# Optimization experiments

Measured on AMD Instinct MI355X. Metric: run time of the kernel, lower is better.

## Reference

```python
import jax, jax.numpy as jnp
import numpy as np

N = 50000   # nodes
E = 400000  # edges
R = 35      # num_relations
B = 12      # num_bases
C = 128     # hidden_conv_dim (heads=1)
T = 4       # node types: load, gen, load_gen, ext
HL = 38     # hidden_lin_dim
OUT = 2


def setup_inputs() -> dict:
    key = jax.random.key(0)
    ks = jax.random.split(key, 24)
    s = 0.1  # param scale
    inp = {
        'x': jax.random.normal(ks[0], (N, 2), jnp.float32),
        'edge_index': jax.random.randint(ks[1], (2, E), 0, N, jnp.int32),
        'edge_type': jax.random.randint(ks[2], (E,), 0, R, jnp.int32),
        'edge_attr': jax.random.normal(ks[3], (E, 2), jnp.float32),
        'node_type': jax.random.randint(ks[4], (N,), 0, T, jnp.int32),
        'basis': jax.random.normal(ks[5], (B, 2, C), jnp.float32) * s,
        'att_rel': jax.random.normal(ks[6], (R, B), jnp.float32) * s,
        'q_att': jax.random.normal(ks[7], (C, 1), jnp.float32) * s,
        'k_att': jax.random.normal(ks[8], (C, 1), jnp.float32) * s,
        'e_att': jax.random.normal(ks[9], (C, 1), jnp.float32) * s,
        'lin_edge_W': jax.random.normal(ks[10], (2, C), jnp.float32) * s,
        'conv_bias': jax.random.normal(ks[11], (C,), jnp.float32) * s,
        'lin0_W': jax.random.normal(ks[12], (T, C, HL), jnp.float32) * s,
        'lin0_b': jax.random.normal(ks[13], (T, HL), jnp.float32) * s,
        'lin1_W': jax.random.normal(ks[14], (T, HL, HL), jnp.float32) * s,
        'lin1_b': jax.random.normal(ks[15], (T, HL), jnp.float32) * s,
        'lin2_W': jax.random.normal(ks[16], (T, HL, HL), jnp.float32) * s,
        'lin2_b': jax.random.normal(ks[17], (T, HL), jnp.float32) * s,
        'fin_W': jax.random.normal(ks[18], (T, HL, OUT), jnp.float32) * s,
        'fin_b': jax.random.normal(ks[19], (T, OUT), jnp.float32) * s,
    }
    return inp


def _segment_softmax(alpha, dst, n):
    # PyG softmax: max is detached, eps=1e-16 on the denominator
    amax = jax.lax.stop_gradient(jax.ops.segment_max(alpha, dst, num_segments=n))
    ex = jnp.exp(alpha - amax[dst])
    den = jax.ops.segment_sum(ex, dst, num_segments=n) + 1e-16
    return ex / den[dst]


def _per_type_linear(xv, W, b, t):
    # apply node-type-specific Linear: [N,d] x [T,d,h] -> pick row type
    y = jnp.einsum('nd,tdh->nth', xv, W)              # [N,T,h]
    y = jnp.take_along_axis(y, t[:, None, None], axis=1)[:, 0]
    return y + b[t]


def reference(x, edge_index, edge_type, edge_attr, node_type,
              basis, att_rel, q_att, k_att, e_att, lin_edge_W, conv_bias,
              lin0_W, lin0_b, lin1_W, lin1_b, lin2_W, lin2_b, fin_W, fin_b):
    n = x.shape[0]
    src, dst = edge_index[0], edge_index[1]
    # RGATConv with basis decomposition: per-relation weight [R, in=2, C]
    w = jnp.einsum('rb,bio->rio', att_rel, basis)
    w_e = w[edge_type]                                 # [E,2,C] edge gather
    out_i = jnp.einsum('ei,eic->ec', x[dst], w_e)      # [E,C]
    out_j = jnp.einsum('ei,eic->ec', x[src], w_e)      # [E,C]
    ke = (edge_attr @ lin_edge_W) @ e_att              # [E,1]
    alpha = out_i @ q_att + out_j @ k_att + ke         # additive self-attention
    alpha = jax.nn.leaky_relu(alpha, 0.2)
    alpha = _segment_softmax(alpha, dst, n)            # across-relation segment softmax
    msg = alpha * out_j                                # heads=1 -> [E,C]
    agg = jax.ops.segment_sum(msg, dst, num_segments=n) + conv_bias
    h = jax.nn.leaky_relu(agg, 0.2)                    # forward activation (dropout: eval)
    t = node_type
    h = _per_type_linear(jax.nn.relu(h), lin0_W, lin0_b, t)
    h = _per_type_linear(jax.nn.relu(h), lin1_W, lin1_b, t)
    h = _per_type_linear(jax.nn.relu(h), lin2_W, lin2_b, t)
    out = _per_type_linear(h, fin_W, fin_b, t)         # [N,2]
    # load nodes (type 0): second output passes through abs
    load_out = jnp.concatenate([out[:, :1], jnp.abs(out[:, 1:2])], axis=1)
    return jnp.where((t == 0)[:, None], load_out, out)
```

## Files before the change

### kernel.cpp

```cpp
#include <hip/hip_runtime.h>
#include <math.h>

#define N_NODES 50000
#define N_EDGES 400000
#define R_REL   35
#define B_BASES 12
#define C_DIM   128
#define HL_DIM  38
#define RI2     70
#define BI2     24
#define NP      50304
#define NB_HIST 196
#define NBUCK   786
#define EPB     1024
#define NEB     391
#define CAP     704

#define OFF_WQ     8960
#define OFF_WK     9030
#define OFF_LE     9100
#define OFF_META   9104
#define OFF_HBLK   9120
#define OFF_PERM   10688
#define OFF_INV    60688
#define OFF_ECUR   110992
#define OFF_EREC   111780
#define OFF_W0P    2325156
#define OFF_W1P    2345636
#define OFF_W2P    2351716

#define ST    0
#define SB    4760
#define HH    0
#define Y0T   0
#define Y1T   3264
#define Y2T   0
#define SM_DINV 8192
#define SM_FW   8256
#define SM_FB   8332
#define LDS_FLOATS 8334

__global__ __launch_bounds__(256) void k_hist(const int* __restrict__ node_type,
                                              float* __restrict__ ws) {
    int b = blockIdx.x, tid = threadIdx.x;
    if (b >= NB_HIST) {
        for (int i = tid; i < NBUCK; i += 256) ((int*)(ws + OFF_ECUR))[i] = 0;
        return;
    }
    __shared__ int lh[4];
    if (tid < 4) lh[tid] = 0;
    __syncthreads();
    int i = b * 256 + tid;
    if (i < N_NODES) atomicAdd(&lh[node_type[i]], 1);
    __syncthreads();
    if (tid < 4) ((int*)(ws + OFF_HBLK))[b * 4 + tid] = lh[tid];
}

__global__ __launch_bounds__(256) void k_perm2(const int* __restrict__ node_type,
                                               const float* __restrict__ basis,
                                               const float* __restrict__ att_rel,
                                               const float* __restrict__ q_att,
                                               const float* __restrict__ k_att,
                                               const float* __restrict__ e_att,
                                               const float* __restrict__ lin_edge_W,
                                               const float* __restrict__ lin0_W,
                                               const float* __restrict__ lin1_W,
                                               const float* __restrict__ lin2_W,
                                               float* __restrict__ ws) {
    int b = blockIdx.x, tid = threadIdx.x;
    int lane = tid & 63, wv = tid >> 6;
    if (b >= NB_HIST) {
        if (b < NB_HIST + 36) {
            int u = (b - NB_HIST) * 4 + wv;
            if (u < 2 * RI2) {
                int ri = (u < RI2) ? u : (u - RI2);
                int r = ri >> 1, ii = ri & 1;
                const float* av = att_rel + r * B_BASES;
                const float* bs = basis + ii * C_DIM;
                float w1 = 0.f, w2 = 0.f;
                #pragma unroll
                for (int bb = 0; bb < B_BASES; ++bb) {
                    float a = av[bb];
                    w1 += a * bs[bb * 2 * C_DIM + lane];
                    w2 += a * bs[bb * 2 * C_DIM + 64 + lane];
                }
                const float* qk = (u < RI2) ? q_att : k_att;
                float s = w1 * qk[lane] + w2 * qk[64 + lane];
                #pragma unroll
                for (int off = 32; off; off >>= 1) s += __shfl_xor(s, off, 64);
                if (lane == 0) ws[((u < RI2) ? OFF_WQ : OFF_WK) + ri] = s;
            } else if (u < 2 * RI2 + 2) {
                int j = u - 2 * RI2;
                const float* er = lin_edge_W + j * C_DIM;
                float s = er[lane] * e_att[lane] + er[64 + lane] * e_att[64 + lane];
                #pragma unroll
                for (int off = 32; off; off >>= 1) s += __shfl_xor(s, off, 64);
                if (lane == 0) ws[OFF_LE + j] = s;
            }
        } else {
            int g = (b - (NB_HIST + 36)) * 256 + tid;
            for (int idx = g; idx < 4 * C_DIM * HL_DIM; idx += 16 * 256) {
                int tt = idx / (C_DIM * HL_DIM);
                int rem = idx - tt * (C_DIM * HL_DIM);
                int cc = rem / HL_DIM, j = rem - cc * HL_DIM;
                ws[OFF_W0P + tt * (C_DIM * 40) + cc * 40 + j] = lin0_W[idx];
            }
            for (int idx = g; idx < 4 * HL_DIM * HL_DIM; idx += 16 * 256) {
                int tt = idx / (HL_DIM * HL_DIM);
                int rem = idx - tt * (HL_DIM * HL_DIM);
                int cc = rem / HL_DIM, j = rem - cc * HL_DIM;
                ws[OFF_W1P + tt * (HL_DIM * 40) + cc * 40 + j] = lin1_W[idx];
                ws[OFF_W2P + tt * (HL_DIM * 40) + cc * 40 + j] = lin2_W[idx];
            }
        }
        return;
    }

    __shared__ int lh[NB_HIST * 4];
    __shared__ int pre[4], tot[4], basel[4];
    __shared__ int wcnt[4][4];
    const int* hblk = (const int*)(ws + OFF_HBLK);
    for (int i = tid; i < NB_HIST * 4; i += 256) lh[i] = hblk[i];
    __syncthreads();
    if (tid < 4) {
        int run = 0, mypre = 0;
        for (int bb = 0; bb < NB_HIST; ++bb) {
            if (bb == b) mypre = run;
            run += lh[bb * 4 + tid];
        }
        pre[tid] = mypre;
        tot[tid] = run;
    }
    __syncthreads();
    if (tid == 0) {
        int t0 = tot[0], t1 = tot[1], t2 = tot[2];
        int b1 = ((t0 + 63) >> 6) << 6;
        int b2 = b1 + (((t1 + 63) >> 6) << 6);
        int b3 = b2 + (((t2 + 63) >> 6) << 6);
        basel[0] = 0; basel[1] = b1; basel[2] = b2; basel[3] = b3;
        if (b == 0) {
            int* meta = (int*)(ws + OFF_META);
            meta[0] = t0; meta[1] = t1; meta[2] = t2; meta[3] = tot[3];
            meta[4] = 0;  meta[5] = b1; meta[6] = b2; meta[7] = b3;
        }
    }
    __syncthreads();
    int n = b * 256 + tid;
    bool active = n < N_NODES;
    int ty = active ? node_type[n] : -1;
    int myrank = 0;
    #pragma unroll
    for (int t = 0; t < 4; ++t) {
        unsigned long long m = __ballot(ty == t);
        if (lane == 0) wcnt[wv][t] = __popcll(m);
        if (ty == t) myrank = __popcll(m & ((1ULL << lane) - 1ULL));
    }
    __syncthreads();
    if (active) {
        int prew = 0;
        for (int w2 = 0; w2 < wv; ++w2) prew += wcnt[w2][ty];
        int p = basel[ty] + pre[ty] + prew + myrank;
        ((int*)(ws + OFF_PERM))[n] = p;
        ((int*)(ws + OFF_INV))[p] = n;
    }
}

__global__ __launch_bounds__(512) void k_escatter(const float* __restrict__ x,
                                                  const int* __restrict__ edge_index,
                                                  const int* __restrict__ edge_type,
                                                  const float* __restrict__ edge_attr,
                                                  float* __restrict__ ws) {
    __shared__ int hist[NBUCK];
    __shared__ int sbase[NBUCK];
    __shared__ float swq[RI2], swk[RI2], sle[2];
    int tid = threadIdx.x;
    for (int i = tid; i < NBUCK; i += 512) hist[i] = 0;
    if (tid < RI2) { swq[tid] = ws[OFF_WQ + tid]; swk[tid] = ws[OFF_WK + tid]; }
    if (tid < 2) sle[tid] = ws[OFF_LE + tid];
    __syncthreads();

    const int* perm = (const int*)(ws + OFF_PERM);
    int base = blockIdx.x * EPB;
    int   rb[2], rm[2];
    float rex[2], rsx[2], rsy[2];
    #pragma unroll
    for (int k = 0; k < 2; ++k) {
        int e = base + k * 512 + tid;
        rb[k] = -1;
        if (e < N_EDGES) {
            int src = edge_index[e];
            int dst = edge_index[N_EDGES + e];
            int r   = edge_type[e];
            int p   = perm[dst];
            float2 ea = *(const float2*)(edge_attr + 2 * e);
            float2 xs = *(const float2*)(x + 2 * src);
            float2 xd = *(const float2*)(x + 2 * dst);
            float alpha = xd.x * swq[2 * r] + xd.y * swq[2 * r + 1]
                        + xs.x * swk[2 * r] + xs.y * swk[2 * r + 1]
                        + ea.x * sle[0]     + ea.y * sle[1];
            alpha = alpha > 0.f ? alpha : 0.2f * alpha;
            float ex = __expf(alpha);
            rb[k]  = p >> 6;
            rm[k]  = (r << 6) | (p & 63);
            rex[k] = ex;
            rsx[k] = ex * xs.x;
            rsy[k] = ex * xs.y;
            atomicAdd(&hist[rb[k]], 1);
        }
    }
    __syncthreads();
    int* gcur = (int*)(ws + OFF_ECUR);
    for (int i = tid; i < NBUCK; i += 512) {
        int c = hist[i];
        sbase[i] = (c > 0) ? atomicAdd(&gcur[i], c) : 0;
    }
    __syncthreads();
    float4* rec = (float4*)(ws + OFF_EREC);
    #pragma unroll
    for (int k = 0; k < 2; ++k) {
        if (rb[k] >= 0) {
            int slot = atomicAdd(&sbase[rb[k]], 1);
            rec[(size_t)rb[k] * CAP + slot] =
                make_float4(__int_as_float(rm[k]), rex[k], rsx[k], rsy[k]);
        }
    }
}

__global__ __launch_bounds__(256, 4) void k_node(
        const float* __restrict__ ws, const float* __restrict__ basis,
        const float* __restrict__ att_rel, const float* __restrict__ conv_bias,
        const float* __restrict__ lin0_b, const float* __restrict__ lin1_b,
        const float* __restrict__ lin2_b, const float* __restrict__ fin_W,
        const float* __restrict__ fin_b, float* __restrict__ out) {
    __shared__ float L[LDS_FLOATS];
    int tid  = threadIdx.x;
    int lane = tid & 63;
    int wv   = tid >> 6;
    int p0   = blockIdx.x * 64;

    const int* meta = (const int*)(ws + OFF_META);
    int b1 = meta[5], b2 = meta[6], b3 = meta[7];
    int t  = (p0 >= b1) + (p0 >= b2) + (p0 >= b3);
    int bp = meta[4 + t];
    int cnt = meta[t];

    for (int i4 = tid; i4 < (RI2 * 68 + BI2 * 68) / 4; i4 += 256)
        *(float4*)&L[ST + i4 * 4] = make_float4(0.f, 0.f, 0.f, 0.f);
    if (tid < 64) L[SM_DINV + tid] = 0.f;
    if (tid >= 64 && tid < 142) {
        int i = tid - 64;
        if (i < 76) L[SM_FW + i] = fin_W[t * 76 + i];
        else        L[SM_FB + i - 76] = fin_b[t * 2 + i - 76];
    }
    __syncthreads();

    {
        int ecnt = ((const int*)(ws + OFF_ECUR))[blockIdx.x];
        const float4* rec = (const float4*)(ws + OFF_EREC) + (size_t)blockIdx.x * CAP;
        for (int i = tid; i < ecnt; i += 256) {
            float4 v = rec[i];
            int m = __float_as_int(v.x);
            int n = m & 63, r = m >> 6;
            atomicAdd(&L[ST + (2 * r) * 68 + n],     v.z);
            atomicAdd(&L[ST + (2 * r + 1) * 68 + n], v.w);
            atomicAdd(&L[SM_DINV + n],               v.y);
        }
    }
    __syncthreads();
    if (tid < 64) L[SM_DINV + tid] = 1.0f / (L[SM_DINV + tid] + 1e-16f);

    if (tid < 128) {
        int n = tid & 63, ii = tid >> 6;
        float pb[B_BASES];
        #pragma unroll
        for (int bq = 0; bq < B_BASES; ++bq) pb[bq] = 0.f;
        #pragma unroll 5
        for (int r = 0; r < R_REL; ++r) {
            float s = L[ST + (2 * r + ii) * 68 + n];
            #pragma unroll
            for (int bq = 0; bq < B_BASES; ++bq)
                pb[bq] += s * att_rel[r * B_BASES + bq];
        }
        #pragma unroll
        for (int bq = 0; bq < B_BASES; ++bq)
            L[SB + (2 * bq + ii) * 68 + n] = pb[bq];
    }
    __syncthreads();

    int ng = lane & 15, cg_ = lane >> 4;
    int c0 = wv * 32 + cg_ * 8;
    float acc[32];
    #pragma unroll
    for (int i = 0; i < 32; ++i) acc[i] = 0.f;
    #pragma unroll 4
    for (int kk = 0; kk < BI2; ++kk) {
        float4 a4 = *(const float4*)&L[SB + kk * 68 + ng * 4];
        float4 wa = *(const float4*)&basis[kk * 128 + c0];
        float4 wc = *(const float4*)&basis[kk * 128 + c0 + 4];
        float a_[4] = {a4.x, a4.y, a4.z, a4.w};
        float w_[8] = {wa.x, wa.y, wa.z, wa.w, wc.x, wc.y, wc.z, wc.w};
        #pragma unroll
        for (int ni = 0; ni < 4; ++ni)
            #pragma unroll
            for (int ci = 0; ci < 8; ++ci)
                acc[ni * 8 + ci] += a_[ni] * w_[ci];
    }
    __syncthreads();

    {
        float4 dv = *(const float4*)&L[SM_DINV + ng * 4];
        float d_[4] = {dv.x, dv.y, dv.z, dv.w};
        #pragma unroll
        for (int ci = 0; ci < 8; ++ci) {
            float cb = conv_bias[c0 + ci];
            float4 hv;
            float h0 = acc[0 * 8 + ci] * d_[0] + cb;
            float h1 = acc[1 * 8 + ci] * d_[1] + cb;
            float h2 = acc[2 * 8 + ci] * d_[2] + cb;
            float h3 = acc[3 * 8 + ci] * d_[3] + cb;
            hv.x = h0 > 0.f ? h0 : 0.f;
            hv.y = h1 > 0.f ? h1 : 0.f;
            hv.z = h2 > 0.f ? h2 : 0.f;
            hv.w = h3 > 0.f ? h3 : 0.f;
            *(float4*)&L[HH + (c0 + ci) * 64 + ng * 4] = hv;
        }
    }
    __syncthreads();

    int jg = lane >> 4;
    int j0 = wv * 16 + jg * 4;
    const float* W0g = ws + OFF_W0P + t * (C_DIM * 40);
    float acc2[16];
    #pragma unroll
    for (int i = 0; i < 16; ++i) acc2[i] = 0.f;
    if (wv < 3) {
        #pragma unroll 4
        for (int kk = 0; kk < C_DIM; ++kk) {
            float4 a4 = *(const float4*)&L[HH + kk * 64 + ng * 4];
            float4 w4 = *(const float4*)&W0g[kk * 40 + j0];
            float a_[4] = {a4.x, a4.y, a4.z, a4.w};
            float w_[4] = {w4.x, w4.y, w4.z, w4.w};
            #pragma unroll
            for (int ni = 0; ni < 4; ++ni)
                #pragma unroll
                for (int ji = 0; ji < 4; ++ji)
                    acc2[ni * 4 + ji] += a_[ni] * w_[ji];
        }
    }
    __syncthreads();

    if (wv < 3) {
        #pragma unroll
        for (int ji = 0; ji < 4; ++ji) {
            int j = j0 + ji;
            float bb = (j < HL_DIM) ? lin0_b[t * HL_DIM + j] : 0.f;
            float4 yv;
            float y0 = acc2[0 * 4 + ji] + bb;
            float y1 = acc2[1 * 4 + ji] + bb;
            float y2 = acc2[2 * 4 + ji] + bb;
            float y3 = acc2[3 * 4 + ji] + bb;
            yv.x = y0 > 0.f ? y0 : 0.f;
            yv.y = y1 > 0.f ? y1 : 0.f;
            yv.z = y2 > 0.f ? y2 : 0.f;
            yv.w = y3 > 0.f ? y3 : 0.f;
            *(float4*)&L[Y0T + j * 68 + ng * 4] = yv;
        }
    }
    __syncthreads();

    if (wv < 3) {
        const float* W1g = ws + OFF_W1P + t * (HL_DIM * 40);
        float acc3[16];
        #pragma unroll
        for (int i = 0; i < 16; ++i) acc3[i] = 0.f;
        #pragma unroll 2
        for (int kk = 0; kk < HL_DIM; ++kk) {
            float4 a4 = *(const float4*)&L[Y0T + kk * 68 + ng * 4];
            float4 w4 = *(const float4*)&W1g[kk * 40 + j0];
            float a_[4] = {a4.x, a4.y, a4.z, a4.w};
            float w_[4] = {w4.x, w4.y, w4.z, w4.w};
            #pragma unroll
            for (int ni = 0; ni < 4; ++ni)
                #pragma unroll
                for (int ji = 0; ji < 4; ++ji)
                    acc3[ni * 4 + ji] += a_[ni] * w_[ji];
        }
        #pragma unroll
        for (int ji = 0; ji < 4; ++ji) {
            int j = j0 + ji;
            float bb = (j < HL_DIM) ? lin1_b[t * HL_DIM + j] : 0.f;
            float4 yv;
            float y0 = acc3[0 * 4 + ji] + bb;
            float y1 = acc3[1 * 4 + ji] + bb;
            float y2 = acc3[2 * 4 + ji] + bb;
            float y3 = acc3[3 * 4 + ji] + bb;
            yv.x = y0 > 0.f ? y0 : 0.f;
            yv.y = y1 > 0.f ? y1 : 0.f;
            yv.z = y2 > 0.f ? y2 : 0.f;
            yv.w = y3 > 0.f ? y3 : 0.f;
            *(float4*)&L[Y1T + j * 68 + ng * 4] = yv;
        }
    }
    __syncthreads();

    if (wv < 3) {
        const float* W2g = ws + OFF_W2P + t * (HL_DIM * 40);
        float acc4[16];
        #pragma unroll
        for (int i = 0; i < 16; ++i) acc4[i] = 0.f;
        #pragma unroll 2
        for (int kk = 0; kk < HL_DIM; ++kk) {
            float4 a4 = *(const float4*)&L[Y1T + kk * 68 + ng * 4];
            float4 w4 = *(const float4*)&W2g[kk * 40 + j0];
            float a_[4] = {a4.x, a4.y, a4.z, a4.w};
            float w_[4] = {w4.x, w4.y, w4.z, w4.w};
            #pragma unroll
            for (int ni = 0; ni < 4; ++ni)
                #pragma unroll
                for (int ji = 0; ji < 4; ++ji)
                    acc4[ni * 4 + ji] += a_[ni] * w_[ji];
        }
        #pragma unroll
        for (int ji = 0; ji < 4; ++ji) {
            int j = j0 + ji;
            float bb = (j < HL_DIM) ? lin2_b[t * HL_DIM + j] : 0.f;
            float4 yv;
            yv.x = acc4[0 * 4 + ji] + bb;
            yv.y = acc4[1 * 4 + ji] + bb;
            yv.z = acc4[2 * 4 + ji] + bb;
            yv.w = acc4[3 * 4 + ji] + bb;
            *(float4*)&L[Y2T + j * 68 + ng * 4] = yv;
        }
    }
    __syncthreads();

    if (tid < 64) {
        int p = p0 + tid;
        bool valid = (p - bp) < cnt;
        float o0 = L[SM_FB], o1 = L[SM_FB + 1];
        for (int jj = 0; jj < HL_DIM; ++jj) {
            float v = L[Y2T + jj * 68 + tid];
            float2 f = *(const float2*)&L[SM_FW + jj * 2];
            o0 += v * f.x;
            o1 += v * f.y;
        }
        if (t == 0) o1 = fabsf(o1);
        if (valid) {
            int orig = ((const int*)(ws + OFF_INV))[p];
            ((float2*)out)[orig] = make_float2(o0, o1);
        }
    }
}

extern "C" void kernel_launch(void* const* d_in, const int* in_sizes, int n_in,
                              void* d_out, int out_size, void* d_ws, size_t ws_size,
                              hipStream_t stream) {
    const float* x          = (const float*)d_in[0];
    const int*   edge_index = (const int*)  d_in[1];
    const int*   edge_type  = (const int*)  d_in[2];
    const float* edge_attr  = (const float*)d_in[3];
    const int*   node_type  = (const int*)  d_in[4];
    const float* basis      = (const float*)d_in[5];
    const float* att_rel    = (const float*)d_in[6];
    const float* q_att      = (const float*)d_in[7];
    const float* k_att      = (const float*)d_in[8];
    const float* e_att      = (const float*)d_in[9];
    const float* lin_edge_W = (const float*)d_in[10];
    const float* conv_bias  = (const float*)d_in[11];
    const float* lin0_W     = (const float*)d_in[12];
    const float* lin0_b     = (const float*)d_in[13];
    const float* lin1_W     = (const float*)d_in[14];
    const float* lin1_b     = (const float*)d_in[15];
    const float* lin2_W     = (const float*)d_in[16];
    const float* lin2_b     = (const float*)d_in[17];
    const float* fin_W      = (const float*)d_in[18];
    const float* fin_b      = (const float*)d_in[19];

    float* ws  = (float*)d_ws;
    float* out = (float*)d_out;

    k_hist    <<<NB_HIST + 1, 256, 0, stream>>>(node_type, ws);
    k_perm2   <<<NB_HIST + 36 + 16, 256, 0, stream>>>(node_type, basis, att_rel,
                                                      q_att, k_att, e_att, lin_edge_W,
                                                      lin0_W, lin1_W, lin2_W, ws);
    k_escatter<<<NEB, 512, 0, stream>>>(x, edge_index, edge_type, edge_attr, ws);
    k_node    <<<NBUCK, 256, 0, stream>>>(ws, basis, att_rel, conv_bias,
                                          lin0_b, lin1_b, lin2_b, fin_W, fin_b, out);
}
```

Baseline: 161.1 us.

## Fuse four kernels into one persistent kernel with software grid barriers

Merges the histogram, permutation, edge-scatter and node kernels into a single launch of 786 blocks, separated by atomic-counter grid barriers kept in workspace. The barrier counters and bucket cursors are zeroed by a memset before the launch. The edge scatter now uses 256-thread blocks handling 512 edges each, so all 786 blocks take part. The aim is to remove launch gaps between the stages. In exchange it relies on all 786 blocks being co-resident, otherwise the kernel deadlocks, and it pays for spin-wait barriers plus an extra memset.

```diff
diff --git a/kernel.cpp b/kernel.cpp
--- a/kernel.cpp
+++ b/kernel.cpp
@@ -12,8 +12,8 @@
 #define NP      50304
 #define NB_HIST 196
 #define NBUCK   786
-#define EPB     1024
-#define NEB     391
+#define NEB2    782
+#define EPB2    512
 #define CAP     704
 
 #define OFF_WQ     8960
@@ -21,6 +21,7 @@
 #define OFF_LE     9100
 #define OFF_META   9104
 #define OFF_HBLK   9120
+#define OFF_BAR    9920
 #define OFF_PERM   10688
 #define OFF_INV    60688
 #define OFF_ECUR   110992
@@ -40,414 +41,425 @@
 #define SM_FB   8332
 #define LDS_FLOATS 8334
 
-__global__ __launch_bounds__(256) void k_hist(const int* __restrict__ node_type,
-                                              float* __restrict__ ws) {
-    int b = blockIdx.x, tid = threadIdx.x;
-    if (b >= NB_HIST) {
-        for (int i = tid; i < NBUCK; i += 256) ((int*)(ws + OFF_ECUR))[i] = 0;
-        return;
+__device__ __forceinline__ void gridbar(float* ws, int idx) {
+    __syncthreads();
+    if (threadIdx.x == 0) {
+        int* bar = (int*)(ws + OFF_BAR) + idx * 16;
+        __threadfence();
+        atomicAdd(bar, 1);
+        while (__hip_atomic_load(bar, __ATOMIC_RELAXED,
+                                 __HIP_MEMORY_SCOPE_AGENT) < NBUCK)
+            __builtin_amdgcn_s_sleep(2);
+        __threadfence();
     }
-    __shared__ int lh[4];
-    if (tid < 4) lh[tid] = 0;
     __syncthreads();
-    int i = b * 256 + tid;
-    if (i < N_NODES) atomicAdd(&lh[node_type[i]], 1);
-    __syncthreads();
-    if (tid < 4) ((int*)(ws + OFF_HBLK))[b * 4 + tid] = lh[tid];
 }
 
-__global__ __launch_bounds__(256) void k_perm2(const int* __restrict__ node_type,
-                                               const float* __restrict__ basis,
-                                               const float* __restrict__ att_rel,
-                                               const float* __restrict__ q_att,
-                                               const float* __restrict__ k_att,
-                                               const float* __restrict__ e_att,
-                                               const float* __restrict__ lin_edge_W,
-                                               const float* __restrict__ lin0_W,
-                                               const float* __restrict__ lin1_W,
-                                               const float* __restrict__ lin2_W,
-                                               float* __restrict__ ws) {
+__global__ __launch_bounds__(256, 4) void k_fused(
+        const float* __restrict__ x,
+        const int* __restrict__ edge_index,
+        const int* __restrict__ edge_type,
+        const float* __restrict__ edge_attr,
+        const int* __restrict__ node_type,
+        const float* __restrict__ basis,
+        const float* __restrict__ att_rel,
+        const float* __restrict__ q_att,
+        const float* __restrict__ k_att,
+        const float* __restrict__ e_att,
+        const float* __restrict__ lin_edge_W,
+        const float* __restrict__ conv_bias,
+        const float* __restrict__ lin0_W,
+        const float* __restrict__ lin0_b,
+        const float* __restrict__ lin1_W,
+        const float* __restrict__ lin1_b,
+        const float* __restrict__ lin2_W,
+        const float* __restrict__ lin2_b,
+        const float* __restrict__ fin_W,
+        const float* __restrict__ fin_b,
+        float* __restrict__ ws,
+        float* __restrict__ out) {
+    __shared__ float L[LDS_FLOATS];
     int b = blockIdx.x, tid = threadIdx.x;
     int lane = tid & 63, wv = tid >> 6;
-    if (b >= NB_HIST) {
-        if (b < NB_HIST + 36) {
-            int u = (b - NB_HIST) * 4 + wv;
-            if (u < 2 * RI2) {
-                int ri = (u < RI2) ? u : (u - RI2);
-                int r = ri >> 1, ii = ri & 1;
-                const float* av = att_rel + r * B_BASES;
-                const float* bs = basis + ii * C_DIM;
-                float w1 = 0.f, w2 = 0.f;
+
+    if (b < NB_HIST) {
+        int* lh = (int*)L;
+        if (tid < 4) lh[tid] = 0;
+        __syncthreads();
+        int i = b * 256 + tid;
+        if (i < N_NODES) atomicAdd(&lh[node_type[i]], 1);
+        __syncthreads();
+        if (tid < 4) ((int*)(ws + OFF_HBLK))[b * 4 + tid] = lh[tid];
+    } else if (b < NB_HIST + 36) {
+        int u = (b - NB_HIST) * 4 + wv;
+        if (u < 2 * RI2) {
+            int ri = (u < RI2) ? u : (u - RI2);
+            int r = ri >> 1, ii = ri & 1;
+            const float* av = att_rel + r * B_BASES;
+            const float* bs = basis + ii * C_DIM;
+            float w1 = 0.f, w2 = 0.f;
+            #pragma unroll
+            for (int bb = 0; bb < B_BASES; ++bb) {
+                float a = av[bb];
+                w1 += a * bs[bb * 2 * C_DIM + lane];
+                w2 += a * bs[bb * 2 * C_DIM + 64 + lane];
+            }
+            const float* qk = (u < RI2) ? q_att : k_att;
+            float s = w1 * qk[lane] + w2 * qk[64 + lane];
+            #pragma unroll
+            for (int off = 32; off; off >>= 1) s += __shfl_xor(s, off, 64);
+            if (lane == 0) ws[((u < RI2) ? OFF_WQ : OFF_WK) + ri] = s;
+        } else if (u < 2 * RI2 + 2) {
+            int j = u - 2 * RI2;
+            const float* er = lin_edge_W + j * C_DIM;
+            float s = er[lane] * e_att[lane] + er[64 + lane] * e_att[64 + lane];
+            #pragma unroll
+            for (int off = 32; off; off >>= 1) s += __shfl_xor(s, off, 64);
+            if (lane == 0) ws[OFF_LE + j] = s;
+        }
+    } else if (b < NB_HIST + 36 + 16) {
+        int g = (b - (NB_HIST + 36)) * 256 + tid;
+        for (int idx = g; idx < 4 * C_DIM * HL_DIM; idx += 16 * 256) {
+            int tt = idx / (C_DIM * HL_DIM);
+            int rem = idx - tt * (C_DIM * HL_DIM);
+            int cc = rem / HL_DIM, j = rem - cc * HL_DIM;
+            ws[OFF_W0P + tt * (C_DIM * 40) + cc * 40 + j] = lin0_W[idx];
+        }
+        for (int idx = g; idx < 4 * HL_DIM * HL_DIM; idx += 16 * 256) {
+            int tt = idx / (HL_DIM * HL_DIM);
+            int rem = idx - tt * (HL_DIM * HL_DIM);
+            int cc = rem / HL_DIM, j = rem - cc * HL_DIM;
+            ws[OFF_W1P + tt * (HL_DIM * 40) + cc * 40 + j] = lin1_W[idx];
+            ws[OFF_W2P + tt * (HL_DIM * 40) + cc * 40 + j] = lin2_W[idx];
+        }
+    }
+    gridbar(ws, 0);
+
+    if (b < NB_HIST) {
+        int* lh    = (int*)L;
+        int* pre   = lh + NB_HIST * 4;
+        int* tot   = pre + 4;
+        int* basel = tot + 4;
+        int (*wcnt)[4] = (int(*)[4])(basel + 4);
+        const int* hblk = (const int*)(ws + OFF_HBLK);
+        for (int i = tid; i < NB_HIST * 4; i += 256) lh[i] = hblk[i];
+        __syncthreads();
+        if (tid < 4) {
+            int run = 0, mypre = 0;
+            for (int bb = 0; bb < NB_HIST; ++bb) {
+                if (bb == b) mypre = run;
+                run += lh[bb * 4 + tid];
+            }
+            pre[tid] = mypre;
+            tot[tid] = run;
+        }
+        __syncthreads();
+        if (tid == 0) {
+            int t0 = tot[0], t1 = tot[1], t2 = tot[2];
+            int b1 = ((t0 + 63) >> 6) << 6;
+            int b2 = b1 + (((t1 + 63) >> 6) << 6);
+            int b3 = b2 + (((t2 + 63) >> 6) << 6);
+            basel[0] = 0; basel[1] = b1; basel[2] = b2; basel[3] = b3;
+            if (b == 0) {
+                int* meta = (int*)(ws + OFF_META);
+                meta[0] = t0; meta[1] = t1; meta[2] = t2; meta[3] = tot[3];
+                meta[4] = 0;  meta[5] = b1; meta[6] = b2; meta[7] = b3;
+            }
+        }
+        __syncthreads();
+        int n = b * 256 + tid;
+        bool active = n < N_NODES;
+        int ty = active ? node_type[n] : -1;
+        int myrank = 0;
+        #pragma unroll
+        for (int t = 0; t < 4; ++t) {
+            unsigned long long m = __ballot(ty == t);
+            if (lane == 0) wcnt[wv][t] = __popcll(m);
+            if (ty == t) myrank = __popcll(m & ((1ULL << lane) - 1ULL));
+        }
+        __syncthreads();
+        if (active) {
+            int prew = 0;
+            for (int w2 = 0; w2 < wv; ++w2) prew += wcnt[w2][ty];
+            int p = basel[ty] + pre[ty] + prew + myrank;
+            ((int*)(ws + OFF_PERM))[n] = p;
+            ((int*)(ws + OFF_INV))[p] = n;
+        }
+    }
+    gridbar(ws, 1);
+
+    if (b < NEB2) {
+        int* hist  = (int*)L;
+        int* sbase = hist + NBUCK;
+        float* swq = L + 2 * NBUCK;
+        float* swk = swq + RI2;
+        float* sle = swk + RI2;
+        for (int i = tid; i < NBUCK; i += 256) hist[i] = 0;
+        if (tid < RI2) { swq[tid] = ws[OFF_WQ + tid]; swk[tid] = ws[OFF_WK + tid]; }
+        if (tid < 2) sle[tid] = ws[OFF_LE + tid];
+        __syncthreads();
+
+        const int* perm = (const int*)(ws + OFF_PERM);
+        int base = b * EPB2;
+        int   rb[2], rm[2];
+        float rex[2], rsx[2], rsy[2];
+        #pragma unroll
+        for (int k = 0; k < 2; ++k) {
+            int e = base + k * 256 + tid;
+            rb[k] = -1;
+            if (e < N_EDGES) {
+                int src = edge_index[e];
+                int dst = edge_index[N_EDGES + e];
+                int r   = edge_type[e];
+                int p   = perm[dst];
+                float2 ea = *(const float2*)(edge_attr + 2 * e);
+                float2 xs = *(const float2*)(x + 2 * src);
+                float2 xd = *(const float2*)(x + 2 * dst);
+                float alpha = xd.x * swq[2 * r] + xd.y * swq[2 * r + 1]
+                            + xs.x * swk[2 * r] + xs.y * swk[2 * r + 1]
+                            + ea.x * sle[0]     + ea.y * sle[1];
+                alpha = alpha > 0.f ? alpha : 0.2f * alpha;
+                float ex = __expf(alpha);
+                rb[k]  = p >> 6;
+                rm[k]  = (r << 6) | (p & 63);
+                rex[k] = ex;
+                rsx[k] = ex * xs.x;
+                rsy[k] = ex * xs.y;
+                atomicAdd(&hist[rb[k]], 1);
+            }
+        }
+        __syncthreads();
+        int* gcur = (int*)(ws + OFF_ECUR);
+        for (int i = tid; i < NBUCK; i += 256) {
+            int c = hist[i];
+            sbase[i] = (c > 0) ? atomicAdd(&gcur[i], c) : 0;
+        }
+        __syncthreads();
+        float4* rec = (float4*)(ws + OFF_EREC);
+        #pragma unroll
+        for (int k = 0; k < 2; ++k) {
+            if (rb[k] >= 0) {
+                int slot = atomicAdd(&sbase[rb[k]], 1);
+                rec[(size_t)rb[k] * CAP + slot] =
+                    make_float4(__int_as_float(rm[k]), rex[k], rsx[k], rsy[k]);
+            }
+        }
+    }
+    gridbar(ws, 2);
+
+    {
+        int p0 = b * 64;
+        const int* meta = (const int*)(ws + OFF_META);
+        int b1 = meta[5], b2 = meta[6], b3 = meta[7];
+        int t  = (p0 >= b1) + (p0 >= b2) + (p0 >= b3);
+        int bp = meta[4 + t];
+        int cnt = meta[t];
+
+        for (int i4 = tid; i4 < (RI2 * 68 + BI2 * 68) / 4; i4 += 256)
+            *(float4*)&L[ST + i4 * 4] = make_float4(0.f, 0.f, 0.f, 0.f);
+        if (tid < 64) L[SM_DINV + tid] = 0.f;
+        if (tid >= 64 && tid < 142) {
+            int i = tid - 64;
+            if (i < 76) L[SM_FW + i] = fin_W[t * 76 + i];
+            else        L[SM_FB + i - 76] = fin_b[t * 2 + i - 76];
+        }
+        __syncthreads();
+
+        {
+            int ecnt = ((const int*)(ws + OFF_ECUR))[b];
+            const float4* rec = (const float4*)(ws + OFF_EREC) + (size_t)b * CAP;
+            for (int i = tid; i < ecnt; i += 256) {
+                float4 v = rec[i];
+                int m = __float_as_int(v.x);
+                int n = m & 63, r = m >> 6;
+                atomicAdd(&L[ST + (2 * r) * 68 + n],     v.z);
+                atomicAdd(&L[ST + (2 * r + 1) * 68 + n], v.w);
+                atomicAdd(&L[SM_DINV + n],               v.y);
+            }
+        }
+        __syncthreads();
+        if (tid < 64) L[SM_DINV + tid] = 1.0f / (L[SM_DINV + tid] + 1e-16f);
+
+        if (tid < 128) {
+            int n = tid & 63, ii = tid >> 6;
+            float pb[B_BASES];
+            #pragma unroll
+            for (int bq = 0; bq < B_BASES; ++bq) pb[bq] = 0.f;
+            #pragma unroll 5
+            for (int r = 0; r < R_REL; ++r) {
+                float s = L[ST + (2 * r + ii) * 68 + n];
                 #pragma unroll
-                for (int bb = 0; bb < B_BASES; ++bb) {
-                    float a = av[bb];
-                    w1 += a * bs[bb * 2 * C_DIM + lane];
-                    w2 += a * bs[bb * 2 * C_DIM + 64 + lane];
-                }
-                const float* qk = (u < RI2) ? q_att : k_att;
-                float s = w1 * qk[lane] + w2 * qk[64 + lane];
-                #pragma unroll
-                for (int off = 32; off; off >>= 1) s += __shfl_xor(s, off, 64);
-                if (lane == 0) ws[((u < RI2) ? OFF_WQ : OFF_WK) + ri] = s;
-            } else if (u < 2 * RI2 + 2) {
-                int j = u - 2 * RI2;
-                const float* er = lin_edge_W + j * C_DIM;
-                float s = er[lane] * e_att[lane] + er[64 + lane] * e_att[64 + lane];
-                #pragma unroll
-                for (int off = 32; off; off >>= 1) s += __shfl_xor(s, off, 64);
-                if (lane == 0) ws[OFF_LE + j] = s;
-            }
-        } else {
-            int g = (b - (NB_HIST + 36)) * 256 + tid;
-            for (int idx = g; idx < 4 * C_DIM * HL_DIM; idx += 16 * 256) {
-                int tt = idx / (C_DIM * HL_DIM);
-                int rem = idx - tt * (C_DIM * HL_DIM);
-                int cc = rem / HL_DIM, j = rem - cc * HL_DIM;
-                ws[OFF_W0P + tt * (C_DIM * 40) + cc * 40 + j] = lin0_W[idx];
-            }
-            for (int idx = g; idx < 4 * HL_DIM * HL_DIM; idx += 16 * 256) {
-                int tt = idx / (HL_DIM * HL_DIM);
-                int rem = idx - tt * (HL_DIM * HL_DIM);
-                int cc = rem / HL_DIM, j = rem - cc * HL_DIM;
-                ws[OFF_W1P + tt * (HL_DIM * 40) + cc * 40 + j] = lin1_W[idx];
-                ws[OFF_W2P + tt * (HL_DIM * 40) + cc * 40 + j] = lin2_W[idx];
-            }
-        }
-        return;
-    }
-
-    __shared__ int lh[NB_HIST * 4];
-    __shared__ int pre[4], tot[4], basel[4];
-    __shared__ int wcnt[4][4];
-    const int* hblk = (const int*)(ws + OFF_HBLK);
-    for (int i = tid; i < NB_HIST * 4; i += 256) lh[i] = hblk[i];
-    __syncthreads();
-    if (tid < 4) {
-        int run = 0, mypre = 0;
-        for (int bb = 0; bb < NB_HIST; ++bb) {
-            if (bb == b) mypre = run;
-            run += lh[bb * 4 + tid];
-        }
-        pre[tid] = mypre;
-        tot[tid] = run;
-    }
-    __syncthreads();
-    if (tid == 0) {
-        int t0 = tot[0], t1 = tot[1], t2 = tot[2];
-        int b1 = ((t0 + 63) >> 6) << 6;
-        int b2 = b1 + (((t1 + 63) >> 6) << 6);
-        int b3 = b2 + (((t2 + 63) >> 6) << 6);
-        basel[0] = 0; basel[1] = b1; basel[2] = b2; basel[3] = b3;
-        if (b == 0) {
-            int* meta = (int*)(ws + OFF_META);
-            meta[0] = t0; meta[1] = t1; meta[2] = t2; meta[3] = tot[3];
-            meta[4] = 0;  meta[5] = b1; meta[6] = b2; meta[7] = b3;
-        }
-    }
-    __syncthreads();
-    int n = b * 256 + tid;
-    bool active = n < N_NODES;
-    int ty = active ? node_type[n] : -1;
-    int myrank = 0;
-    #pragma unroll
-    for (int t = 0; t < 4; ++t) {
-        unsigned long long m = __ballot(ty == t);
-        if (lane == 0) wcnt[wv][t] = __popcll(m);
-        if (ty == t) myrank = __popcll(m & ((1ULL << lane) - 1ULL));
-    }
-    __syncthreads();
-    if (active) {
-        int prew = 0;
-        for (int w2 = 0; w2 < wv; ++w2) prew += wcnt[w2][ty];
-        int p = basel[ty] + pre[ty] + prew + myrank;
-        ((int*)(ws + OFF_PERM))[n] = p;
-        ((int*)(ws + OFF_INV))[p] = n;
-    }
-}
-
-__global__ __launch_bounds__(512) void k_escatter(const float* __restrict__ x,
-                                                  const int* __restrict__ edge_index,
-                                                  const int* __restrict__ edge_type,
-                                                  const float* __restrict__ edge_attr,
-                                                  float* __restrict__ ws) {
-    __shared__ int hist[NBUCK];
-    __shared__ int sbase[NBUCK];
-    __shared__ float swq[RI2], swk[RI2], sle[2];
-    int tid = threadIdx.x;
-    for (int i = tid; i < NBUCK; i += 512) hist[i] = 0;
-    if (tid < RI2) { swq[tid] = ws[OFF_WQ + tid]; swk[tid] = ws[OFF_WK + tid]; }
-    if (tid < 2) sle[tid] = ws[OFF_LE + tid];
-    __syncthreads();
-
-    const int* perm = (const int*)(ws + OFF_PERM);
-    int base = blockIdx.x * EPB;
-    int   rb[2], rm[2];
-    float rex[2], rsx[2], rsy[2];
-    #pragma unroll
-    for (int k = 0; k < 2; ++k) {
-        int e = base + k * 512 + tid;
-        rb[k] = -1;
-        if (e < N_EDGES) {
-            int src = edge_index[e];
-            int dst = edge_index[N_EDGES + e];
-            int r   = edge_type[e];
-            int p   = perm[dst];
-            float2 ea = *(const float2*)(edge_attr + 2 * e);
-            float2 xs = *(const float2*)(x + 2 * src);
-            float2 xd = *(const float2*)(x + 2 * dst);
-            float alpha = xd.x * swq[2 * r] + xd.y * swq[2 * r + 1]
-                        + xs.x * swk[2 * r] + xs.y * swk[2 * r + 1]
-                        + ea.x * sle[0]     + ea.y * sle[1];
-            alpha = alpha > 0.f ? alpha : 0.2f * alpha;
-            float ex = __expf(alpha);
-            rb[k]  = p >> 6;
-            rm[k]  = (r << 6) | (p & 63);
-            rex[k] = ex;
-            rsx[k] = ex * xs.x;
-            rsy[k] = ex * xs.y;
-            atomicAdd(&hist[rb[k]], 1);
-        }
-    }
-    __syncthreads();
-    int* gcur = (int*)(ws + OFF_ECUR);
-    for (int i = tid; i < NBUCK; i += 512) {
-        int c = hist[i];
-        sbase[i] = (c > 0) ? atomicAdd(&gcur[i], c) : 0;
-    }
-    __syncthreads();
-    float4* rec = (float4*)(ws + OFF_EREC);
-    #pragma unroll
-    for (int k = 0; k < 2; ++k) {
-        if (rb[k] >= 0) {
-            int slot = atomicAdd(&sbase[rb[k]], 1);
-            rec[(size_t)rb[k] * CAP + slot] =
-                make_float4(__int_as_float(rm[k]), rex[k], rsx[k], rsy[k]);
-        }
-    }
-}
-
-__global__ __launch_bounds__(256, 4) void k_node(
-        const float* __restrict__ ws, const float* __restrict__ basis,
-        const float* __restrict__ att_rel, const float* __restrict__ conv_bias,
-        const float* __restrict__ lin0_b, const float* __restrict__ lin1_b,
-        const float* __restrict__ lin2_b, const float* __restrict__ fin_W,
-        const float* __restrict__ fin_b, float* __restrict__ out) {
-    __shared__ float L[LDS_FLOATS];
-    int tid  = threadIdx.x;
-    int lane = tid & 63;
-    int wv   = tid >> 6;
-    int p0   = blockIdx.x * 64;
-
-    const int* meta = (const int*)(ws + OFF_META);
-    int b1 = meta[5], b2 = meta[6], b3 = meta[7];
-    int t  = (p0 >= b1) + (p0 >= b2) + (p0 >= b3);
-    int bp = meta[4 + t];
-    int cnt = meta[t];
-
-    for (int i4 = tid; i4 < (RI2 * 68 + BI2 * 68) / 4; i4 += 256)
-        *(float4*)&L[ST + i4 * 4] = make_float4(0.f, 0.f, 0.f, 0.f);
-    if (tid < 64) L[SM_DINV + tid] = 0.f;
-    if (tid >= 64 && tid < 142) {
-        int i = tid - 64;
-        if (i < 76) L[SM_FW + i] = fin_W[t * 76 + i];
-        else        L[SM_FB + i - 76] = fin_b[t * 2 + i - 76];
-    }
-    __syncthreads();
-
-    {
-        int ecnt = ((const int*)(ws + OFF_ECUR))[blockIdx.x];
-        const float4* rec = (const float4*)(ws + OFF_EREC) + (size_t)blockIdx.x * CAP;
-        for (int i = tid; i < ecnt; i += 256) {
-            float4 v = rec[i];
-            int m = __float_as_int(v.x);
-            int n = m & 63, r = m >> 6;
-            atomicAdd(&L[ST + (2 * r) * 68 + n],     v.z);
-            atomicAdd(&L[ST + (2 * r + 1) * 68 + n], v.w);
-            atomicAdd(&L[SM_DINV + n],               v.y);
-        }
-    }
-    __syncthreads();
-    if (tid < 64) L[SM_DINV + tid] = 1.0f / (L[SM_DINV + tid] + 1e-16f);
-
-    if (tid < 128) {
-        int n = tid & 63, ii = tid >> 6;
-        float pb[B_BASES];
+                for (int bq = 0; bq < B_BASES; ++bq)
+                    pb[bq] += s * att_rel[r * B_BASES + bq];
+            }
+            #pragma unroll
+            for (int bq = 0; bq < B_BASES; ++bq)
+                L[SB + (2 * bq + ii) * 68 + n] = pb[bq];
+        }
+        __syncthreads();
+
+        int ng = lane & 15, cg_ = lane >> 4;
+        int c0 = wv * 32 + cg_ * 8;
+        float acc[32];
         #pragma unroll
-        for (int bq = 0; bq < B_BASES; ++bq) pb[bq] = 0.f;
-        #pragma unroll 5
-        for (int r = 0; r < R_REL; ++r) {
-            float s = L[ST + (2 * r + ii) * 68 + n];
-            #pragma unroll
-            for (int bq = 0; bq < B_BASES; ++bq)
-                pb[bq] += s * att_rel[r * B_BASES + bq];
-        }
-        #pragma unroll
-        for (int bq = 0; bq < B_BASES; ++bq)
-            L[SB + (2 * bq + ii) * 68 + n] = pb[bq];
-    }
-    __syncthreads();
-
-    int ng = lane & 15, cg_ = lane >> 4;
-    int c0 = wv * 32 + cg_ * 8;
-    float acc[32];
-    #pragma unroll
-    for (int i = 0; i < 32; ++i) acc[i] = 0.f;
-    #pragma unroll 4
-    for (int kk = 0; kk < BI2; ++kk) {
-        float4 a4 = *(const float4*)&L[SB + kk * 68 + ng * 4];
-        float4 wa = *(const float4*)&basis[kk * 128 + c0];
-        float4 wc = *(const float4*)&basis[kk * 128 + c0 + 4];
-        float a_[4] = {a4.x, a4.y, a4.z, a4.w};
-        float w_[8] = {wa.x, wa.y, wa.z, wa.w, wc.x, wc.y, wc.z, wc.w};
-        #pragma unroll
-        for (int ni = 0; ni < 4; ++ni)
-            #pragma unroll
-            for (int ci = 0; ci < 8; ++ci)
-                acc[ni * 8 + ci] += a_[ni] * w_[ci];
-    }
-    __syncthreads();
-
-    {
-        float4 dv = *(const float4*)&L[SM_DINV + ng * 4];
-        float d_[4] = {dv.x, dv.y, dv.z, dv.w};
-        #pragma unroll
-        for (int ci = 0; ci < 8; ++ci) {
-            float cb = conv_bias[c0 + ci];
-            float4 hv;
-            float h0 = acc[0 * 8 + ci] * d_[0] + cb;
-            float h1 = acc[1 * 8 + ci] * d_[1] + cb;
-            float h2 = acc[2 * 8 + ci] * d_[2] + cb;
-            float h3 = acc[3 * 8 + ci] * d_[3] + cb;
-            hv.x = h0 > 0.f ? h0 : 0.f;
-            hv.y = h1 > 0.f ? h1 : 0.f;
-            hv.z = h2 > 0.f ? h2 : 0.f;
-            hv.w = h3 > 0.f ? h3 : 0.f;
-            *(float4*)&L[HH + (c0 + ci) * 64 + ng * 4] = hv;
-        }
-    }
-    __syncthreads();
-
-    int jg = lane >> 4;
-    int j0 = wv * 16 + jg * 4;
-    const float* W0g = ws + OFF_W0P + t * (C_DIM * 40);
-    float acc2[16];
-    #pragma unroll
-    for (int i = 0; i < 16; ++i) acc2[i] = 0.f;
-    if (wv < 3) {
+        for (int i = 0; i < 32; ++i) acc[i] = 0.f;
         #pragma unroll 4
-        for (int kk = 0; kk < C_DIM; ++kk) {
-            float4 a4 = *(const float4*)&L[HH + kk * 64 + ng * 4];
-            float4 w4 = *(const float4*)&W0g[kk * 40 + j0];
+        for (int kk = 0; kk < BI2; ++kk) {
+            float4 a4 = *(const float4*)&L[SB + kk * 68 + ng * 4];
+            float4 wa = *(const float4*)&basis[kk * 128 + c0];
+            float4 wc = *(const float4*)&basis[kk * 128 + c0 + 4];
             float a_[4] = {a4.x, a4.y, a4.z, a4.w};
-            float w_[4] = {w4.x, w4.y, w4.z, w4.w};
+            float w_[8] = {wa.x, wa.y, wa.z, wa.w, wc.x, wc.y, wc.z, wc.w};
             #pragma unroll
             for (int ni = 0; ni < 4; ++ni)
                 #pragma unroll
-                for (int ji = 0; ji < 4; ++ji)
-                    acc2[ni * 4 + ji] += a_[ni] * w_[ji];
-        }
-    }
-    __syncthreads();
-
-    if (wv < 3) {
+                for (int ci = 0; ci < 8; ++ci)
+                    acc[ni * 8 + ci] += a_[ni] * w_[ci];
+        }
+        __syncthreads();
+
+        {
+            float4 dv = *(const float4*)&L[SM_DINV + ng * 4];
+            float d_[4] = {dv.x, dv.y, dv.z, dv.w};
+            #pragma unroll
+            for (int ci = 0; ci < 8; ++ci) {
+                float cb = conv_bias[c0 + ci];
+                float4 hv;
+                float h0 = acc[0 * 8 + ci] * d_[0] + cb;
+                float h1 = acc[1 * 8 + ci] * d_[1] + cb;
+                float h2 = acc[2 * 8 + ci] * d_[2] + cb;
+                float h3 = acc[3 * 8 + ci] * d_[3] + cb;
+                hv.x = h0 > 0.f ? h0 : 0.f;
+                hv.y = h1 > 0.f ? h1 : 0.f;
+                hv.z = h2 > 0.f ? h2 : 0.f;
+                hv.w = h3 > 0.f ? h3 : 0.f;
+                *(float4*)&L[HH + (c0 + ci) * 64 + ng * 4] = hv;
+            }
+        }
+        __syncthreads();
+
+        int jg = lane >> 4;
+        int j0 = wv * 16 + jg * 4;
+        const float* W0g = ws + OFF_W0P + t * (C_DIM * 40);
+        float acc2[16];
         #pragma unroll
-        for (int ji = 0; ji < 4; ++ji) {
-            int j = j0 + ji;
-            float bb = (j < HL_DIM) ? lin0_b[t * HL_DIM + j] : 0.f;
-            float4 yv;
-            float y0 = acc2[0 * 4 + ji] + bb;
-            float y1 = acc2[1 * 4 + ji] + bb;
-            float y2 = acc2[2 * 4 + ji] + bb;
-            float y3 = acc2[3 * 4 + ji] + bb;
-            yv.x = y0 > 0.f ? y0 : 0.f;
-            yv.y = y1 > 0.f ? y1 : 0.f;
-            yv.z = y2 > 0.f ? y2 : 0.f;
-            yv.w = y3 > 0.f ? y3 : 0.f;
-            *(float4*)&L[Y0T + j * 68 + ng * 4] = yv;
-        }
-    }
-    __syncthreads();
-
-    if (wv < 3) {
-        const float* W1g = ws + OFF_W1P + t * (HL_DIM * 40);
-        float acc3[16];
-        #pragma unroll
-        for (int i = 0; i < 16; ++i) acc3[i] = 0.f;
-        #pragma unroll 2
-        for (int kk = 0; kk < HL_DIM; ++kk) {
-            float4 a4 = *(const float4*)&L[Y0T + kk * 68 + ng * 4];
-            float4 w4 = *(const float4*)&W1g[kk * 40 + j0];
-            float a_[4] = {a4.x, a4.y, a4.z, a4.w};
-            float w_[4] = {w4.x, w4.y, w4.z, w4.w};
-            #pragma unroll
-            for (int ni = 0; ni < 4; ++ni)
+        for (int i = 0; i < 16; ++i) acc2[i] = 0.f;
+        if (wv < 3) {
+            #pragma unroll 4
+            for (int kk = 0; kk < C_DIM; ++kk) {
+                float4 a4 = *(const float4*)&L[HH + kk * 64 + ng * 4];
+                float4 w4 = *(const float4*)&W0g[kk * 40 + j0];
+                float a_[4] = {a4.x, a4.y, a4.z, a4.w};
+                float w_[4] = {w4.x, w4.y, w4.z, w4.w};
                 #pragma unroll
-                for (int ji = 0; ji < 4; ++ji)
-                    acc3[ni * 4 + ji] += a_[ni] * w_[ji];
-        }
-        #pragma unroll
-        for (int ji = 0; ji < 4; ++ji) {
-            int j = j0 + ji;
-            float bb = (j < HL_DIM) ? lin1_b[t * HL_DIM + j] : 0.f;
-            float4 yv;
-            float y0 = acc3[0 * 4 + ji] + bb;
-            float y1 = acc3[1 * 4 + ji] + bb;
-            float y2 = acc3[2 * 4 + ji] + bb;
-            float y3 = acc3[3 * 4 + ji] + bb;
-            yv.x = y0 > 0.f ? y0 : 0.f;
-            yv.y = y1 > 0.f ? y1 : 0.f;
-            yv.z = y2 > 0.f ? y2 : 0.f;
-            yv.w = y3 > 0.f ? y3 : 0.f;
-            *(float4*)&L[Y1T + j * 68 + ng * 4] = yv;
-        }
-    }
-    __syncthreads();
-
-    if (wv < 3) {
-        const float* W2g = ws + OFF_W2P + t * (HL_DIM * 40);
-        float acc4[16];
-        #pragma unroll
-        for (int i = 0; i < 16; ++i) acc4[i] = 0.f;
-        #pragma unroll 2
-        for (int kk = 0; kk < HL_DIM; ++kk) {
-            float4 a4 = *(const float4*)&L[Y1T + kk * 68 + ng * 4];
-            float4 w4 = *(const float4*)&W2g[kk * 40 + j0];
-            float a_[4] = {a4.x, a4.y, a4.z, a4.w};
-            float w_[4] = {w4.x, w4.y, w4.z, w4.w};
-            #pragma unroll
-            for (int ni = 0; ni < 4; ++ni)
+                for (int ni = 0; ni < 4; ++ni)
+                    #pragma unroll
+                    for (int ji = 0; ji < 4; ++ji)
+                        acc2[ni * 4 + ji] += a_[ni] * w_[ji];
+            }
+        }
+        __syncthreads();
+
+        if (wv < 3) {
+            #pragma unroll
+            for (int ji = 0; ji < 4; ++ji) {
+                int j = j0 + ji;
+                float bb = (j < HL_DIM) ? lin0_b[t * HL_DIM + j] : 0.f;
+                float4 yv;
+                float y0 = acc2[0 * 4 + ji] + bb;
+                float y1 = acc2[1 * 4 + ji] + bb;
+                float y2 = acc2[2 * 4 + ji] + bb;
+                float y3 = acc2[3 * 4 + ji] + bb;
+                yv.x = y0 > 0.f ? y0 : 0.f;
+                yv.y = y1 > 0.f ? y1 : 0.f;
+                yv.z = y2 > 0.f ? y2 : 0.f;
+                yv.w = y3 > 0.f ? y3 : 0.f;
+                *(float4*)&L[Y0T + j * 68 + ng * 4] = yv;
+            }
+        }
+        __syncthreads();
+
+        if (wv < 3) {
+            const float* W1g = ws + OFF_W1P + t * (HL_DIM * 40);
+            float acc3[16];
+            #pragma unroll
+            for (int i = 0; i < 16; ++i) acc3[i] = 0.f;
+            #pragma unroll 2
+            for (int kk = 0; kk < HL_DIM; ++kk) {
+                float4 a4 = *(const float4*)&L[Y0T + kk * 68 + ng * 4];
+                float4 w4 = *(const float4*)&W1g[kk * 40 + j0];
+                float a_[4] = {a4.x, a4.y, a4.z, a4.w};
+                float w_[4] = {w4.x, w4.y, w4.z, w4.w};
                 #pragma unroll
-                for (int ji = 0; ji < 4; ++ji)
-                    acc4[ni * 4 + ji] += a_[ni] * w_[ji];
-        }
-        #pragma unroll
-        for (int ji = 0; ji < 4; ++ji) {
-            int j = j0 + ji;
-            float bb = (j < HL_DIM) ? lin2_b[t * HL_DIM + j] : 0.f;
-            float4 yv;
-            yv.x = acc4[0 * 4 + ji] + bb;
-            yv.y = acc4[1 * 4 + ji] + bb;
-            yv.z = acc4[2 * 4 + ji] + bb;
-            yv.w = acc4[3 * 4 + ji] + bb;
-            *(float4*)&L[Y2T + j * 68 + ng * 4] = yv;
-        }
-    }
-    __syncthreads();
-
-    if (tid < 64) {
-        int p = p0 + tid;
-        bool valid = (p - bp) < cnt;
-        float o0 = L[SM_FB], o1 = L[SM_FB + 1];
-        for (int jj = 0; jj < HL_DIM; ++jj) {
-            float v = L[Y2T + jj * 68 + tid];
-            float2 f = *(const float2*)&L[SM_FW + jj * 2];
-            o0 += v * f.x;
-            o1 += v * f.y;
-        }
-        if (t == 0) o1 = fabsf(o1);
-        if (valid) {
-            int orig = ((const int*)(ws + OFF_INV))[p];
-            ((float2*)out)[orig] = make_float2(o0, o1);
+                for (int ni = 0; ni < 4; ++ni)
+                    #pragma unroll
+                    for (int ji = 0; ji < 4; ++ji)
+                        acc3[ni * 4 + ji] += a_[ni] * w_[ji];
+            }
+            #pragma unroll
+            for (int ji = 0; ji < 4; ++ji) {
+                int j = j0 + ji;
+                float bb = (j < HL_DIM) ? lin1_b[t * HL_DIM + j] : 0.f;
+                float4 yv;
+                float y0 = acc3[0 * 4 + ji] + bb;
+                float y1 = acc3[1 * 4 + ji] + bb;
+                float y2 = acc3[2 * 4 + ji] + bb;
+                float y3 = acc3[3 * 4 + ji] + bb;
+                yv.x = y0 > 0.f ? y0 : 0.f;
+                yv.y = y1 > 0.f ? y1 : 0.f;
+                yv.z = y2 > 0.f ? y2 : 0.f;
+                yv.w = y3 > 0.f ? y3 : 0.f;
+                *(float4*)&L[Y1T + j * 68 + ng * 4] = yv;
+            }
+        }
+        __syncthreads();
+
+        if (wv < 3) {
+            const float* W2g = ws + OFF_W2P + t * (HL_DIM * 40);
+            float acc4[16];
+            #pragma unroll
+            for (int i = 0; i < 16; ++i) acc4[i] = 0.f;
+            #pragma unroll 2
+            for (int kk = 0; kk < HL_DIM; ++kk) {
+                float4 a4 = *(const float4*)&L[Y1T + kk * 68 + ng * 4];
+                float4 w4 = *(const float4*)&W2g[kk * 40 + j0];
+                float a_[4] = {a4.x, a4.y, a4.z, a4.w};
+                float w_[4] = {w4.x, w4.y, w4.z, w4.w};
+                #pragma unroll
+                for (int ni = 0; ni < 4; ++ni)
+                    #pragma unroll
+                    for (int ji = 0; ji < 4; ++ji)
+                        acc4[ni * 4 + ji] += a_[ni] * w_[ji];
+            }
+            #pragma unroll
+            for (int ji = 0; ji < 4; ++ji) {
+                int j = j0 + ji;
+                float bb = (j < HL_DIM) ? lin2_b[t * HL_DIM + j] : 0.f;
+                float4 yv;
+                yv.x = acc4[0 * 4 + ji] + bb;
+                yv.y = acc4[1 * 4 + ji] + bb;
+                yv.z = acc4[2 * 4 + ji] + bb;
+                yv.w = acc4[3 * 4 + ji] + bb;
+                *(float4*)&L[Y2T + j * 68 + ng * 4] = yv;
+            }
+        }
+        __syncthreads();
+
+        if (tid < 64) {
+            int p = p0 + tid;
+            bool valid = (p - bp) < cnt;
+            float o0 = L[SM_FB], o1 = L[SM_FB + 1];
+            for (int jj = 0; jj < HL_DIM; ++jj) {
+                float v = L[Y2T + jj * 68 + tid];
+                float2 f = *(const float2*)&L[SM_FW + jj * 2];
+                o0 += v * f.x;
+                o1 += v * f.y;
+            }
+            if (t == 0) o1 = fabsf(o1);
+            if (valid) {
+                int orig = ((const int*)(ws + OFF_INV))[p];
+                ((float2*)out)[orig] = make_float2(o0, o1);
+            }
         }
     }
 }
@@ -479,11 +491,12 @@
     float* ws  = (float*)d_ws;
     float* out = (float*)d_out;
 
-    k_hist    <<<NB_HIST + 1, 256, 0, stream>>>(node_type, ws);
-    k_perm2   <<<NB_HIST + 36 + 16, 256, 0, stream>>>(node_type, basis, att_rel,
-                                                      q_att, k_att, e_att, lin_edge_W,
-                                                      lin0_W, lin1_W, lin2_W, ws);
-    k_escatter<<<NEB, 512, 0, stream>>>(x, edge_index, edge_type, edge_attr, ws);
-    k_node    <<<NBUCK, 256, 0, stream>>>(ws, basis, att_rel, conv_bias,
-                                          lin0_b, lin1_b, lin2_b, fin_W, fin_b, out);
+    hipMemsetAsync((char*)d_ws + (size_t)OFF_BAR * 4, 0,
+                   (size_t)(OFF_EREC - OFF_BAR) * 4, stream);
+
+    k_fused<<<NBUCK, 256, 0, stream>>>(x, edge_index, edge_type, edge_attr,
+                                       node_type, basis, att_rel, q_att, k_att,
+                                       e_att, lin_edge_W, conv_bias,
+                                       lin0_W, lin0_b, lin1_W, lin1_b,
+                                       lin2_W, lin2_b, fin_W, fin_b, ws, out);
 }
```

Result: slower. 398.1 us (+147.1%).
